# Optimization experiments

Hardware: AMD Instinct MI355X
Metric: run time of the kernel (lower is better)

Reference implementation:

```python
import jax, jax.numpy as jnp
import numpy as np

DIM = 128
B, N = 4, 4096


def setup_inputs() -> dict:
    key = jax.random.key(0)
    k1, k2, k3 = jax.random.split(key, 3)
    return {
        "key": jax.random.normal(k1, (B, N, DIM), dtype=jnp.float32),
        "query": jax.random.normal(k2, (B, N, DIM), dtype=jnp.float32),
        "value": jax.random.normal(k3, (B, N, DIM), dtype=jnp.float32),
    }


def reference(key, query, value):
    # score[b, i, j] = <query[b, i], key[b, j]> / sqrt(dim)
    inv_sqrt_dim = 1.0 / jnp.sqrt(jnp.float32(DIM))
    score = jnp.einsum("bqd,bkd->bqk", query, key) * inv_sqrt_dim
    attn = jax.nn.softmax(score, axis=-1)
    context = jnp.einsum("bqk,bkd->bqd", attn, value)
    return (context, attn)
```

## Files before the change

kernel.cpp:

```cpp
#include <hip/hip_runtime.h>
#include <hip/hip_bf16.h>

#define BDIM 4
#define NSEQ 4096
#define DHEAD 128
#define SCALE 0.08838834764831845f

typedef __bf16 bf16x8 __attribute__((ext_vector_type(8)));
typedef float f32x4 __attribute__((ext_vector_type(4)));

__device__ __forceinline__ unsigned short f2bf(float f){
    return __builtin_bit_cast(unsigned short, (__bf16)f);
}
__device__ __forceinline__ unsigned long long pack4(float4 u){
    return (unsigned long long)f2bf(u.x)
         | ((unsigned long long)f2bf(u.y) << 16)
         | ((unsigned long long)f2bf(u.z) << 32)
         | ((unsigned long long)f2bf(u.w) << 48);
}
__device__ __forceinline__ void gload_lds16(const void* g, void* l){
    __builtin_amdgcn_global_load_lds(
        (const __attribute__((address_space(1))) unsigned int*)g,
        (__attribute__((address_space(3))) unsigned int*)l, 16, 0, 0);
}

extern "C" __global__ __launch_bounds__(256, 4)
void attn_stats(const float* __restrict__ K, const float* __restrict__ Q,
                float* __restrict__ pbase, int pstride)
{
    __shared__ __align__(16) char Klds[64 * 256];

    const int bid = blockIdx.x;
    const int ks  = bid & 3;
    const int rt  = (bid >> 2) & 63;
    const int b   = bid >> 8;
    const int tid = threadIdx.x;
    const int lane = tid & 63;
    const int w    = tid >> 6;
    const int g    = lane >> 4;
    const int c    = lane & 15;
    const int rowbase = rt * 64;

    const float* qrow = Q + ((size_t)b * NSEQ + rowbase + w * 16 + c) * DHEAD;
    bf16x8 qf[4];
#pragma unroll
    for (int kk = 0; kk < 4; kk++) {
        const float4* p0 = (const float4*)(qrow + g * 8 + kk * 32);
        float4 u = p0[0], v = p0[1];
        bf16x8 t;
        t[0] = (__bf16)(u.x * SCALE); t[1] = (__bf16)(u.y * SCALE);
        t[2] = (__bf16)(u.z * SCALE); t[3] = (__bf16)(u.w * SCALE);
        t[4] = (__bf16)(v.x * SCALE); t[5] = (__bf16)(v.y * SCALE);
        t[6] = (__bf16)(v.z * SCALE); t[7] = (__bf16)(v.w * SCALE);
        qf[kk] = t;
    }

    float m[4], l[4];
#pragma unroll
    for (int r = 0; r < 4; r++) { m[r] = -1e30f; l[r] = 0.0f; }

    const int f  = tid & 31;
    const int r0 = tid >> 5;

    for (int kt = 0; kt < 16; kt++) {
        const float* ktile = K + ((size_t)b * NSEQ + ks * 1024 + kt * 64) * DHEAD;
#pragma unroll
        for (int i = 0; i < 8; i++) {
            int r = r0 + i * 8;
            float4 u = *(const float4*)(ktile + (size_t)r * DHEAD + f * 4);
            *(unsigned long long*)(Klds + r * 256 + ((f * 8) ^ ((r & 7) << 4))) = pack4(u);
        }
        __syncthreads();

        f32x4 acc[4];
#pragma unroll
        for (int n = 0; n < 4; n++) acc[n] = (f32x4){0.f, 0.f, 0.f, 0.f};
#pragma unroll
        for (int n = 0; n < 4; n++) {
            int row = n * 16 + c;
#pragma unroll
            for (int kk = 0; kk < 4; kk++) {
                bf16x8 kf = *(const bf16x8*)(Klds + row * 256 +
                                ((g * 16 + kk * 64) ^ ((row & 7) << 4)));
                acc[n] = __builtin_amdgcn_mfma_f32_16x16x32_bf16(qf[kk], kf, acc[n], 0, 0, 0);
            }
        }

#pragma unroll
        for (int r = 0; r < 4; r++) {
            float t = fmaxf(fmaxf(acc[0][r], acc[1][r]), fmaxf(acc[2][r], acc[3][r]));
            t = fmaxf(t, __shfl_xor(t, 1));
            t = fmaxf(t, __shfl_xor(t, 2));
            t = fmaxf(t, __shfl_xor(t, 4));
            t = fmaxf(t, __shfl_xor(t, 8));
            float mn = fmaxf(m[r], t);
            float sc = __expf(m[r] - mn);
            float ps = __expf(acc[0][r] - mn) + __expf(acc[1][r] - mn)
                     + __expf(acc[2][r] - mn) + __expf(acc[3][r] - mn);
            ps += __shfl_xor(ps, 1);
            ps += __shfl_xor(ps, 2);
            ps += __shfl_xor(ps, 4);
            ps += __shfl_xor(ps, 8);
            l[r] = l[r] * sc + ps;
            m[r] = mn;
        }
        __syncthreads();
    }

    if (c == 0) {
#pragma unroll
        for (int r = 0; r < 4; r++) {
            size_t row = rowbase + w * 16 + g * 4 + r;
            float* p = pbase + ((size_t)b * NSEQ + row) * pstride + ks * 2;
            p[0] = m[r];
            p[1] = l[r];
        }
    }
}

extern "C" __global__ __launch_bounds__(256, 4)
void repack(const float* __restrict__ K, const float* __restrict__ V,
            char* __restrict__ ws)
{
    const int bid = blockIdx.x;
    const int T = bid & 63;
    const int b = bid >> 6;
    const int tid = threadIdx.x;

    char* Kp = ws + ((size_t)(b * 64 + T) << 14);
    char* Vp = ws + (4u << 20) + ((size_t)(b * 64 + T) << 14);
    const float* Ks = K + ((size_t)b * NSEQ + T * 64) * DHEAD;
    const float* Vs = V + ((size_t)b * NSEQ + T * 64) * DHEAD;

#pragma unroll
    for (int i = 0; i < 4; i++) {
        int u = tid + 256 * i;
        int row = u >> 4, j = u & 15;
        const float* s = Ks + (size_t)row * DHEAD + (j ^ (row & 7)) * 8;
        float4 a = *(const float4*)s;
        float4 bq = *(const float4*)(s + 4);
        ulonglong2 wv;
        wv.x = pack4(a);
        wv.y = pack4(bq);
        *(ulonglong2*)(Kp + row * 256 + j * 16) = wv;
    }
#pragma unroll
    for (int i = 0; i < 4; i++) {
        int u = tid + 256 * i;
        int d = u >> 3, jj = u & 7;
        int k0 = (jj ^ (d & 7)) * 8;
        float v0 = Vs[(size_t)(k0 + 0) * DHEAD + d];
        float v1 = Vs[(size_t)(k0 + 1) * DHEAD + d];
        float v2 = Vs[(size_t)(k0 + 2) * DHEAD + d];
        float v3 = Vs[(size_t)(k0 + 3) * DHEAD + d];
        float v4 = Vs[(size_t)(k0 + 4) * DHEAD + d];
        float v5 = Vs[(size_t)(k0 + 5) * DHEAD + d];
        float v6 = Vs[(size_t)(k0 + 6) * DHEAD + d];
        float v7 = Vs[(size_t)(k0 + 7) * DHEAD + d];
        ulonglong2 wv;
        wv.x = (unsigned long long)f2bf(v0)
             | ((unsigned long long)f2bf(v1) << 16)
             | ((unsigned long long)f2bf(v2) << 32)
             | ((unsigned long long)f2bf(v3) << 48);
        wv.y = (unsigned long long)f2bf(v4)
             | ((unsigned long long)f2bf(v5) << 16)
             | ((unsigned long long)f2bf(v6) << 32)
             | ((unsigned long long)f2bf(v7) << 48);
        *(ulonglong2*)(Vp + d * 128 + jj * 16) = wv;
    }
}

extern "C" __global__ __launch_bounds__(512, 4)
void attn_final2(const char* __restrict__ ws, const float* __restrict__ Q,
                 float* __restrict__ out)
{
    __shared__ __align__(16) char LDS[73728];

    const int bid = blockIdx.x;
    const int ks  = bid & 1;
    const int rt  = (bid >> 1) & 63;
    const int b   = bid >> 7;
    const int tid = threadIdx.x;
    const int rowbase = rt * 64;
    const int lane = tid & 63;
    const int w    = tid >> 6;
    const int rw   = w & 3;
    const int kh   = w >> 2;
    const int g    = lane >> 4;
    const int c    = lane & 15;

    float* ctxOut = out;
    float* attn   = out + (size_t)BDIM * NSEQ * DHEAD;
    const float* pbase = (const float*)(ws + (8u << 20));

    char* Plds = LDS + 65536 + rw * 2048;

    float Cq;
    {
        const float* prow = pbase + ((size_t)b * NSEQ + rowbase + rw * 16 + c) * 8;
        float4 p0 = *(const float4*)prow;
        float4 p1 = *(const float4*)(prow + 4);
        float M = fmaxf(fmaxf(p0.x, p0.z), fmaxf(p1.x, p1.z));
        float L = p0.y * __expf(p0.x - M) + p0.w * __expf(p0.z - M)
                + p1.y * __expf(p1.x - M) + p1.w * __expf(p1.z - M);
        Cq = M + __logf(L);
    }

    const float* qrow = Q + ((size_t)b * NSEQ + rowbase + rw * 16 + c) * DHEAD;
    bf16x8 qf[4];
#pragma unroll
    for (int kk = 0; kk < 4; kk++) {
        const float4* p0 = (const float4*)(qrow + g * 8 + kk * 32);
        float4 u = p0[0], v = p0[1];
        bf16x8 tt;
        tt[0] = (__bf16)(u.x * SCALE); tt[1] = (__bf16)(u.y * SCALE);
        tt[2] = (__bf16)(u.z * SCALE); tt[3] = (__bf16)(u.w * SCALE);
        tt[4] = (__bf16)(v.x * SCALE); tt[5] = (__bf16)(v.y * SCALE);
        tt[6] = (__bf16)(v.z * SCALE); tt[7] = (__bf16)(v.w * SCALE);
        qf[kk] = tt;
    }

    f32x4 ctx[8];
#pragma unroll
    for (int n2 = 0; n2 < 8; n2++) ctx[n2] = (f32x4){0.f, 0.f, 0.f, 0.f};

    const char* Kg  = ws + ((size_t)(b * 64 + ks * 32) << 14);
    const char* Vg  = ws + (4u << 20) + ((size_t)(b * 64 + ks * 32) << 14);
    const int o0 = tid * 16, o1 = (tid + 512) * 16;

    gload_lds16(Kg + o0, LDS + o0);
    gload_lds16(Kg + o1, LDS + o1);
    gload_lds16(Vg + o0, LDS + 32768 + o0);
    gload_lds16(Vg + o1, LDS + 32768 + o1);

    for (int kt = 0; kt < 32; kt++) {
        __builtin_amdgcn_s_barrier();
        __builtin_amdgcn_sched_barrier(0);
        if (kt < 31) {
            const char* kg = Kg + ((size_t)(kt + 1) << 14);
            const char* vg = Vg + ((size_t)(kt + 1) << 14);
            char* kb = LDS + (((kt + 1) & 1) << 14);
            char* vb = LDS + 32768 + (((kt + 1) & 1) << 14);
            gload_lds16(kg + o0, kb + o0);
            gload_lds16(kg + o1, kb + o1);
            gload_lds16(vg + o0, vb + o0);
            gload_lds16(vg + o1, vb + o1);
            asm volatile("s_waitcnt vmcnt(4)" ::: "memory");
        } else {
            asm volatile("s_waitcnt vmcnt(0)" ::: "memory");
        }
        __builtin_amdgcn_s_barrier();
        __builtin_amdgcn_sched_barrier(0);

        char* Kl = LDS + ((kt & 1) << 14);
        char* Vl = LDS + 32768 + ((kt & 1) << 14);

        f32x4 sacc[2];
#pragma unroll
        for (int nt = 0; nt < 2; nt++) sacc[nt] = (f32x4){0.f, 0.f, 0.f, 0.f};
        __builtin_amdgcn_s_setprio(1);
#pragma unroll
        for (int nt = 0; nt < 2; nt++) {
            int row = kh * 32 + nt * 16 + c;
#pragma unroll
            for (int kk = 0; kk < 4; kk++) {
                bf16x8 kf = *(const bf16x8*)(Kl + row * 256 +
                                ((g * 16 + kk * 64) ^ ((row & 7) << 4)));
                sacc[nt] = __builtin_amdgcn_mfma_f32_16x16x32_bf16(kf, qf[kk], sacc[nt], 0, 0, 0);
            }
        }
        __builtin_amdgcn_s_setprio(0);

        const int col0 = ks * 2048 + kt * 64;
        float* arow = attn + ((size_t)b * NSEQ + rowbase + rw * 16 + c) * NSEQ
                    + col0 + kh * 32;
#pragma unroll
        for (int nt = 0; nt < 2; nt++) {
            float4 pv;
            pv.x = __expf(sacc[nt][0] - Cq);
            pv.y = __expf(sacc[nt][1] - Cq);
            pv.z = __expf(sacc[nt][2] - Cq);
            pv.w = __expf(sacc[nt][3] - Cq);
            *(float4*)(arow + nt * 16 + g * 4) = pv;
            *(unsigned long long*)(Plds + c * 128 +
                ((kh * 64 + nt * 32 + g * 8) ^ ((c & 7) << 4))) = pack4(pv);
        }
        asm volatile("s_waitcnt lgkmcnt(0)" ::: "memory");
        __builtin_amdgcn_sched_barrier(0);

        bf16x8 pf = *(const bf16x8*)(Plds + c * 128 +
                        ((kh * 64 + g * 16) ^ ((c & 7) << 4)));

        __builtin_amdgcn_s_setprio(1);
#pragma unroll
        for (int n2 = 0; n2 < 8; n2++) {
            int d = n2 * 16 + c;
            bf16x8 vf = *(const bf16x8*)(Vl + d * 128 +
                            ((kh * 64 + g * 16) ^ ((d & 7) << 4)));
            ctx[n2] = __builtin_amdgcn_mfma_f32_16x16x32_bf16(pf, vf, ctx[n2], 0, 0, 0);
        }
        __builtin_amdgcn_s_setprio(0);
    }

    __syncthreads();

    float* red = (float*)LDS;
    if (kh == 1) {
#pragma unroll
        for (int n2 = 0; n2 < 8; n2++)
#pragma unroll
            for (int r = 0; r < 4; r++)
                red[(rw * 16 + g * 4 + r) * 128 + n2 * 16 + c] = ctx[n2][r];
    }
    __syncthreads();
    if (kh == 0) {
#pragma unroll
        for (int n2 = 0; n2 < 8; n2++)
#pragma unroll
            for (int r = 0; r < 4; r++) {
                size_t row = rowbase + rw * 16 + g * 4 + r;
                float s = ctx[n2][r] + red[(rw * 16 + g * 4 + r) * 128 + n2 * 16 + c];
                atomicAdd(&ctxOut[((size_t)b * NSEQ + row) * DHEAD + n2 * 16 + c], s);
            }
    }
}

extern "C" __global__ __launch_bounds__(512, 2)
void attn_final_fb(const float* __restrict__ K, const float* __restrict__ Q,
                   const float* __restrict__ V, float* __restrict__ out)
{
    __shared__ __align__(16) char LDS[81920];

    const int bid = blockIdx.x;
    const int rt  = bid & 63;
    const int b   = bid >> 6;
    const int tid = threadIdx.x;
    const int rowbase = rt * 64;
    const int lane = tid & 63;
    const int w    = tid >> 6;
    const int rw   = w & 3;
    const int grp  = w >> 2;
    const int g    = lane >> 4;
    const int c    = lane & 15;
    const int t    = tid & 255;

    float* ctxOut = out;
    float* attn   = out + (size_t)BDIM * NSEQ * DHEAD;

    char* Klds  = LDS + grp * 16384;
    char* Vtlds = LDS + 32768 + grp * 16384;
    char* Plds  = LDS + 65536 + w * 2048;

    float Cq;
    {
        const float* prow = attn + ((size_t)b * NSEQ + rowbase + rw * 16 + c) * NSEQ;
        float4 p0 = *(const float4*)prow;
        float4 p1 = *(const float4*)(prow + 4);
        float M = fmaxf(fmaxf(p0.x, p0.z), fmaxf(p1.x, p1.z));
        float L = p0.y * __expf(p0.x - M) + p0.w * __expf(p0.z - M)
                + p1.y * __expf(p1.x - M) + p1.w * __expf(p1.z - M);
        Cq = M + __logf(L);
    }

    const float* qrow = Q + ((size_t)b * NSEQ + rowbase + rw * 16 + c) * DHEAD;
    bf16x8 qf[4];
#pragma unroll
    for (int kk = 0; kk < 4; kk++) {
        const float4* p0 = (const float4*)(qrow + g * 8 + kk * 32);
        float4 u = p0[0], v = p0[1];
        bf16x8 tt;
        tt[0] = (__bf16)(u.x * SCALE); tt[1] = (__bf16)(u.y * SCALE);
        tt[2] = (__bf16)(u.z * SCALE); tt[3] = (__bf16)(u.w * SCALE);
        tt[4] = (__bf16)(v.x * SCALE); tt[5] = (__bf16)(v.y * SCALE);
        tt[6] = (__bf16)(v.z * SCALE); tt[7] = (__bf16)(v.w * SCALE);
        qf[kk] = tt;
    }

    f32x4 ctx[8];
#pragma unroll
    for (int n2 = 0; n2 < 8; n2++) ctx[n2] = (f32x4){0.f, 0.f, 0.f, 0.f};

    __syncthreads();

    const int fK = t & 31;
    const int rK = t >> 5;
    const int dq = t & 15;
    const int kb = t >> 4;
    const int k0 = kb * 4;
    const int d0 = dq * 2;

    const float* kbase = K + ((size_t)b * NSEQ + grp * 2048) * DHEAD;
    const float* vbase = V + ((size_t)b * NSEQ + grp * 2048) * DHEAD;

    float4 kreg[8];
    float2 vreg[4][4];

#pragma unroll
    for (int i = 0; i < 8; i++)
        kreg[i] = *(const float4*)(kbase + (size_t)(rK + i * 8) * DHEAD + fK * 4);
#pragma unroll
    for (int i = 0; i < 4; i++)
#pragma unroll
        for (int j = 0; j < 4; j++)
            vreg[i][j] = *(const float2*)(vbase + (size_t)(k0 + j) * DHEAD + d0 + 32 * i);

    for (int kt = 0; kt < 32; kt++) {
        __builtin_amdgcn_s_barrier();

#pragma unroll
        for (int i = 0; i < 8; i++) {
            int row = rK + i * 8;
            *(unsigned long long*)(Klds + row * 256 + ((fK * 8) ^ ((row & 7) << 4))) = pack4(kreg[i]);
        }
#pragma unroll
        for (int i = 0; i < 4; i++) {
            int d = d0 + 32 * i;
            unsigned long long rr0 =
                (unsigned long long)f2bf(vreg[i][0].x)
              | ((unsigned long long)f2bf(vreg[i][1].x) << 16)
              | ((unsigned long long)f2bf(vreg[i][2].x) << 32)
              | ((unsigned long long)f2bf(vreg[i][3].x) << 48);
            unsigned long long rr1 =
                (unsigned long long)f2bf(vreg[i][0].y)
              | ((unsigned long long)f2bf(vreg[i][1].y) << 16)
              | ((unsigned long long)f2bf(vreg[i][2].y) << 32)
              | ((unsigned long long)f2bf(vreg[i][3].y) << 48);
            int swz = (d & 7) << 4;
            *(unsigned long long*)(Vtlds + d * 128 + ((k0 * 2) ^ swz)) = rr0;
            *(unsigned long long*)(Vtlds + (d + 1) * 128 + ((k0 * 2) ^ (swz + 16))) = rr1;
        }
        asm volatile("s_waitcnt lgkmcnt(0)" ::: "memory");
        __builtin_amdgcn_s_barrier();

        {
            int kn = (kt + 1) & 31;
            const float* kp = kbase + (size_t)kn * 64 * DHEAD;
            const float* vp = vbase + (size_t)kn * 64 * DHEAD;
#pragma unroll
            for (int i = 0; i < 8; i++)
                kreg[i] = *(const float4*)(kp + (size_t)(rK + i * 8) * DHEAD + fK * 4);
#pragma unroll
            for (int i = 0; i < 4; i++)
#pragma unroll
                for (int j = 0; j < 4; j++)
                    vreg[i][j] = *(const float2*)(vp + (size_t)(k0 + j) * DHEAD + d0 + 32 * i);
        }

        f32x4 sacc[4];
#pragma unroll
        for (int nt = 0; nt < 4; nt++) sacc[nt] = (f32x4){0.f, 0.f, 0.f, 0.f};
        __builtin_amdgcn_s_setprio(1);
#pragma unroll
        for (int nt = 0; nt < 4; nt++) {
            int row = nt * 16 + c;
#pragma unroll
            for (int kk = 0; kk < 4; kk++) {
                bf16x8 kf = *(const bf16x8*)(Klds + row * 256 +
                                ((g * 16 + kk * 64) ^ ((row & 7) << 4)));
                sacc[nt] = __builtin_amdgcn_mfma_f32_16x16x32_bf16(kf, qf[kk], sacc[nt], 0, 0, 0);
            }
        }
        __builtin_amdgcn_s_setprio(0);

        const int col0 = grp * 2048 + kt * 64;
        float* arow = attn + ((size_t)b * NSEQ + rowbase + rw * 16 + c) * NSEQ + col0;
#pragma unroll
        for (int nt = 0; nt < 4; nt++) {
            float4 pv;
            pv.x = __expf(sacc[nt][0] - Cq);
            pv.y = __expf(sacc[nt][1] - Cq);
            pv.z = __expf(sacc[nt][2] - Cq);
            pv.w = __expf(sacc[nt][3] - Cq);
            *(float4*)(arow + nt * 16 + g * 4) = pv;
            *(unsigned long long*)(Plds + c * 128 +
                ((nt * 32 + g * 8) ^ ((c & 7) << 4))) = pack4(pv);
        }
        asm volatile("s_waitcnt lgkmcnt(0)" ::: "memory");
        __builtin_amdgcn_sched_barrier(0);

        bf16x8 pf[2];
#pragma unroll
        for (int kk = 0; kk < 2; kk++)
            pf[kk] = *(const bf16x8*)(Plds + c * 128 +
                        ((kk * 64 + g * 16) ^ ((c & 7) << 4)));

        __builtin_amdgcn_s_setprio(1);
#pragma unroll
        for (int n2 = 0; n2 < 8; n2++) {
            int d = n2 * 16 + c;
#pragma unroll
            for (int kk = 0; kk < 2; kk++) {
                bf16x8 vf = *(const bf16x8*)(Vtlds + d * 128 +
                                ((kk * 64 + g * 16) ^ ((d & 7) << 4)));
                ctx[n2] = __builtin_amdgcn_mfma_f32_16x16x32_bf16(pf[kk], vf, ctx[n2], 0, 0, 0);
            }
        }
        __builtin_amdgcn_s_setprio(0);
    }

    __syncthreads();

    float* red = (float*)LDS;
    if (grp == 1) {
#pragma unroll
        for (int n2 = 0; n2 < 8; n2++)
#pragma unroll
            for (int r = 0; r < 4; r++)
                red[(rw * 16 + g * 4 + r) * 128 + n2 * 16 + c] = ctx[n2][r];
    }
    __syncthreads();
    if (grp == 0) {
#pragma unroll
        for (int n2 = 0; n2 < 8; n2++)
#pragma unroll
            for (int r = 0; r < 4; r++) {
                size_t row = rowbase + rw * 16 + g * 4 + r;
                ctxOut[((size_t)b * NSEQ + row) * DHEAD + n2 * 16 + c] =
                    ctx[n2][r] + red[(rw * 16 + g * 4 + r) * 128 + n2 * 16 + c];
            }
    }
}

extern "C" void kernel_launch(void* const* d_in, const int* in_sizes, int n_in,
                              void* d_out, int out_size, void* d_ws, size_t ws_size,
                              hipStream_t stream)
{
    const float* K = (const float*)d_in[0];
    const float* Q = (const float*)d_in[1];
    const float* V = (const float*)d_in[2];
    float* out  = (float*)d_out;
    float* attn = out + (size_t)BDIM * NSEQ * DHEAD;

    const size_t need = (8u << 20) + (size_t)BDIM * NSEQ * 8 * sizeof(float);
    if (ws_size >= need) {
        char* ws = (char*)d_ws;
        float* pb = (float*)(ws + (8u << 20));
        hipMemsetAsync(out, 0, (size_t)BDIM * NSEQ * DHEAD * sizeof(float), stream);
        attn_stats<<<dim3(4 * 64 * 4), dim3(256), 0, stream>>>(K, Q, pb, 8);
        repack<<<dim3(4 * 64), dim3(256), 0, stream>>>(K, V, ws);
        attn_final2<<<dim3(4 * 64 * 2), dim3(512), 0, stream>>>(ws, Q, out);
    } else {
        attn_stats<<<dim3(4 * 64 * 4), dim3(256), 0, stream>>>(K, Q, attn, NSEQ);
        attn_final_fb<<<dim3(4 * 64), dim3(512), 0, stream>>>(K, Q, V, out);
    }
}
```

Measured before the change: 154.2 us.

## Repack K/V into MFMA fragment order and stream operands directly from global

```diff
diff --git a/kernel.cpp b/kernel.cpp
--- a/kernel.cpp
+++ b/kernel.cpp
@@ -17,11 +17,6 @@
          | ((unsigned long long)f2bf(u.y) << 16)
          | ((unsigned long long)f2bf(u.z) << 32)
          | ((unsigned long long)f2bf(u.w) << 48);
-}
-__device__ __forceinline__ void gload_lds16(const void* g, void* l){
-    __builtin_amdgcn_global_load_lds(
-        (const __attribute__((address_space(1))) unsigned int*)g,
-        (__attribute__((address_space(3))) unsigned int*)l, 16, 0, 0);
 }
 
 extern "C" __global__ __launch_bounds__(256, 4)
@@ -119,8 +114,8 @@
 }
 
 extern "C" __global__ __launch_bounds__(256, 4)
-void repack(const float* __restrict__ K, const float* __restrict__ V,
-            char* __restrict__ ws)
+void repack2(const float* __restrict__ K, const float* __restrict__ V,
+             char* __restrict__ ws)
 {
     const int bid = blockIdx.x;
     const int T = bid & 63;
@@ -135,20 +130,21 @@
 #pragma unroll
     for (int i = 0; i < 4; i++) {
         int u = tid + 256 * i;
-        int row = u >> 4, j = u & 15;
-        const float* s = Ks + (size_t)row * DHEAD + (j ^ (row & 7)) * 8;
+        int t4 = u >> 8, kk = (u >> 6) & 3, g = (u >> 4) & 3, c = u & 15;
+        const float* s = Ks + (size_t)(t4 * 16 + c) * DHEAD + g * 8 + kk * 32;
         float4 a = *(const float4*)s;
         float4 bq = *(const float4*)(s + 4);
         ulonglong2 wv;
         wv.x = pack4(a);
         wv.y = pack4(bq);
-        *(ulonglong2*)(Kp + row * 256 + j * 16) = wv;
+        *(ulonglong2*)(Kp + u * 16) = wv;
     }
 #pragma unroll
     for (int i = 0; i < 4; i++) {
         int u = tid + 256 * i;
-        int d = u >> 3, jj = u & 7;
-        int k0 = (jj ^ (d & 7)) * 8;
+        int n2 = u >> 7, kq = (u >> 6) & 1, g = (u >> 4) & 3, c = u & 15;
+        int d = n2 * 16 + c;
+        int k0 = kq * 32 + g * 8;
         float v0 = Vs[(size_t)(k0 + 0) * DHEAD + d];
         float v1 = Vs[(size_t)(k0 + 1) * DHEAD + d];
         float v2 = Vs[(size_t)(k0 + 2) * DHEAD + d];
@@ -166,15 +162,15 @@
              | ((unsigned long long)f2bf(v5) << 16)
              | ((unsigned long long)f2bf(v6) << 32)
              | ((unsigned long long)f2bf(v7) << 48);
-        *(ulonglong2*)(Vp + d * 128 + jj * 16) = wv;
-    }
-}
-
-extern "C" __global__ __launch_bounds__(512, 4)
-void attn_final2(const char* __restrict__ ws, const float* __restrict__ Q,
+        *(ulonglong2*)(Vp + u * 16) = wv;
+    }
+}
+
+extern "C" __global__ __launch_bounds__(512, 2)
+void attn_stream(const char* __restrict__ ws, const float* __restrict__ Q,
                  float* __restrict__ out)
 {
-    __shared__ __align__(16) char LDS[73728];
+    __shared__ __align__(16) char LDS[32768];
 
     const int bid = blockIdx.x;
     const int ks  = bid & 1;
@@ -184,8 +180,8 @@
     const int rowbase = rt * 64;
     const int lane = tid & 63;
     const int w    = tid >> 6;
-    const int rw   = w & 3;
-    const int kh   = w >> 2;
+    const int kq   = w & 1;
+    const int qh   = w >> 1;
     const int g    = lane >> 4;
     const int c    = lane & 15;
 
@@ -193,11 +189,15 @@
     float* attn   = out + (size_t)BDIM * NSEQ * DHEAD;
     const float* pbase = (const float*)(ws + (8u << 20));
 
-    char* Plds = LDS + 65536 + rw * 2048;
+    char* Pw = LDS + w * 1024;
+    const int swz = ((c >> 2) & 3) << 1;
+    const int pwoff0 = c * 64 + (((0 * 4 + g) ^ swz) << 3);
+    const int pwoff1 = c * 64 + (((1 * 4 + g) ^ swz) << 3);
+    const int proff  = c * 64 + (((2 * g) ^ swz) << 3);
 
     float Cq;
     {
-        const float* prow = pbase + ((size_t)b * NSEQ + rowbase + rw * 16 + c) * 8;
+        const float* prow = pbase + ((size_t)b * NSEQ + rowbase + qh * 16 + c) * 8;
         float4 p0 = *(const float4*)prow;
         float4 p1 = *(const float4*)(prow + 4);
         float M = fmaxf(fmaxf(p0.x, p0.z), fmaxf(p1.x, p1.z));
@@ -206,7 +206,7 @@
         Cq = M + __logf(L);
     }
 
-    const float* qrow = Q + ((size_t)b * NSEQ + rowbase + rw * 16 + c) * DHEAD;
+    const float* qrow = Q + ((size_t)b * NSEQ + rowbase + qh * 16 + c) * DHEAD;
     bf16x8 qf[4];
 #pragma unroll
     for (int kk = 0; kk < 4; kk++) {
@@ -224,102 +224,80 @@
 #pragma unroll
     for (int n2 = 0; n2 < 8; n2++) ctx[n2] = (f32x4){0.f, 0.f, 0.f, 0.f};
 
-    const char* Kg  = ws + ((size_t)(b * 64 + ks * 32) << 14);
-    const char* Vg  = ws + (4u << 20) + ((size_t)(b * 64 + ks * 32) << 14);
-    const int o0 = tid * 16, o1 = (tid + 512) * 16;
-
-    gload_lds16(Kg + o0, LDS + o0);
-    gload_lds16(Kg + o1, LDS + o1);
-    gload_lds16(Vg + o0, LDS + 32768 + o0);
-    gload_lds16(Vg + o1, LDS + 32768 + o1);
-
+    const int loff = g * 256 + c * 16;
+    const char* Kp = ws + ((size_t)(b * 64 + ks * 32) << 14);
+    const char* Vp = ws + (4u << 20) + ((size_t)(b * 64 + ks * 32) << 14);
+    float* arowb = attn + ((size_t)b * NSEQ + rowbase + qh * 16 + c) * NSEQ + ks * 2048;
+
+#pragma unroll 2
     for (int kt = 0; kt < 32; kt++) {
-        __builtin_amdgcn_s_barrier();
-        __builtin_amdgcn_sched_barrier(0);
-        if (kt < 31) {
-            const char* kg = Kg + ((size_t)(kt + 1) << 14);
-            const char* vg = Vg + ((size_t)(kt + 1) << 14);
-            char* kb = LDS + (((kt + 1) & 1) << 14);
-            char* vb = LDS + 32768 + (((kt + 1) & 1) << 14);
-            gload_lds16(kg + o0, kb + o0);
-            gload_lds16(kg + o1, kb + o1);
-            gload_lds16(vg + o0, vb + o0);
-            gload_lds16(vg + o1, vb + o1);
-            asm volatile("s_waitcnt vmcnt(4)" ::: "memory");
-        } else {
-            asm volatile("s_waitcnt vmcnt(0)" ::: "memory");
-        }
-        __builtin_amdgcn_s_barrier();
-        __builtin_amdgcn_sched_barrier(0);
-
-        char* Kl = LDS + ((kt & 1) << 14);
-        char* Vl = LDS + 32768 + ((kt & 1) << 14);
+        const char* kt_base = Kp + ((size_t)kt << 14);
+        const char* vt_base = Vp + ((size_t)kt << 14);
+
+        bf16x8 kf[8];
+#pragma unroll
+        for (int nt = 0; nt < 2; nt++)
+#pragma unroll
+            for (int kk = 0; kk < 4; kk++)
+                kf[nt * 4 + kk] = *(const bf16x8*)(kt_base +
+                    (((kq * 2 + nt) * 4 + kk) << 10) + loff);
+        bf16x8 vf[8];
+#pragma unroll
+        for (int n2 = 0; n2 < 8; n2++)
+            vf[n2] = *(const bf16x8*)(vt_base + ((n2 * 2 + kq) << 10) + loff);
 
         f32x4 sacc[2];
 #pragma unroll
         for (int nt = 0; nt < 2; nt++) sacc[nt] = (f32x4){0.f, 0.f, 0.f, 0.f};
         __builtin_amdgcn_s_setprio(1);
 #pragma unroll
-        for (int nt = 0; nt < 2; nt++) {
-            int row = kh * 32 + nt * 16 + c;
-#pragma unroll
-            for (int kk = 0; kk < 4; kk++) {
-                bf16x8 kf = *(const bf16x8*)(Kl + row * 256 +
-                                ((g * 16 + kk * 64) ^ ((row & 7) << 4)));
-                sacc[nt] = __builtin_amdgcn_mfma_f32_16x16x32_bf16(kf, qf[kk], sacc[nt], 0, 0, 0);
-            }
-        }
+        for (int nt = 0; nt < 2; nt++)
+#pragma unroll
+            for (int kk = 0; kk < 4; kk++)
+                sacc[nt] = __builtin_amdgcn_mfma_f32_16x16x32_bf16(
+                                kf[nt * 4 + kk], qf[kk], sacc[nt], 0, 0, 0);
         __builtin_amdgcn_s_setprio(0);
 
-        const int col0 = ks * 2048 + kt * 64;
-        float* arow = attn + ((size_t)b * NSEQ + rowbase + rw * 16 + c) * NSEQ
-                    + col0 + kh * 32;
-#pragma unroll
-        for (int nt = 0; nt < 2; nt++) {
-            float4 pv;
-            pv.x = __expf(sacc[nt][0] - Cq);
-            pv.y = __expf(sacc[nt][1] - Cq);
-            pv.z = __expf(sacc[nt][2] - Cq);
-            pv.w = __expf(sacc[nt][3] - Cq);
-            *(float4*)(arow + nt * 16 + g * 4) = pv;
-            *(unsigned long long*)(Plds + c * 128 +
-                ((kh * 64 + nt * 32 + g * 8) ^ ((c & 7) << 4))) = pack4(pv);
-        }
+        float* arow = arowb + kt * 64 + kq * 32;
+        float4 pv0, pv1;
+        pv0.x = __expf(sacc[0][0] - Cq); pv0.y = __expf(sacc[0][1] - Cq);
+        pv0.z = __expf(sacc[0][2] - Cq); pv0.w = __expf(sacc[0][3] - Cq);
+        pv1.x = __expf(sacc[1][0] - Cq); pv1.y = __expf(sacc[1][1] - Cq);
+        pv1.z = __expf(sacc[1][2] - Cq); pv1.w = __expf(sacc[1][3] - Cq);
+        *(float4*)(arow + g * 4)      = pv0;
+        *(float4*)(arow + 16 + g * 4) = pv1;
+        *(unsigned long long*)(Pw + pwoff0) = pack4(pv0);
+        *(unsigned long long*)(Pw + pwoff1) = pack4(pv1);
         asm volatile("s_waitcnt lgkmcnt(0)" ::: "memory");
         __builtin_amdgcn_sched_barrier(0);
 
-        bf16x8 pf = *(const bf16x8*)(Plds + c * 128 +
-                        ((kh * 64 + g * 16) ^ ((c & 7) << 4)));
+        bf16x8 pf = *(const bf16x8*)(Pw + proff);
 
         __builtin_amdgcn_s_setprio(1);
 #pragma unroll
-        for (int n2 = 0; n2 < 8; n2++) {
-            int d = n2 * 16 + c;
-            bf16x8 vf = *(const bf16x8*)(Vl + d * 128 +
-                            ((kh * 64 + g * 16) ^ ((d & 7) << 4)));
-            ctx[n2] = __builtin_amdgcn_mfma_f32_16x16x32_bf16(pf, vf, ctx[n2], 0, 0, 0);
-        }
+        for (int n2 = 0; n2 < 8; n2++)
+            ctx[n2] = __builtin_amdgcn_mfma_f32_16x16x32_bf16(pf, vf[n2], ctx[n2], 0, 0, 0);
         __builtin_amdgcn_s_setprio(0);
     }
 
     __syncthreads();
 
     float* red = (float*)LDS;
-    if (kh == 1) {
+    if (kq == 1) {
 #pragma unroll
         for (int n2 = 0; n2 < 8; n2++)
 #pragma unroll
             for (int r = 0; r < 4; r++)
-                red[(rw * 16 + g * 4 + r) * 128 + n2 * 16 + c] = ctx[n2][r];
+                red[(qh * 16 + g * 4 + r) * 128 + n2 * 16 + c] = ctx[n2][r];
     }
     __syncthreads();
-    if (kh == 0) {
+    if (kq == 0) {
 #pragma unroll
         for (int n2 = 0; n2 < 8; n2++)
 #pragma unroll
             for (int r = 0; r < 4; r++) {
-                size_t row = rowbase + rw * 16 + g * 4 + r;
-                float s = ctx[n2][r] + red[(rw * 16 + g * 4 + r) * 128 + n2 * 16 + c];
+                size_t row = rowbase + qh * 16 + g * 4 + r;
+                float s = ctx[n2][r] + red[(qh * 16 + g * 4 + r) * 128 + n2 * 16 + c];
                 atomicAdd(&ctxOut[((size_t)b * NSEQ + row) * DHEAD + n2 * 16 + c], s);
             }
     }
@@ -490,9 +468,9 @@
             int d = n2 * 16 + c;
 #pragma unroll
             for (int kk = 0; kk < 2; kk++) {
-                bf16x8 vf = *(const bf16x8*)(Vtlds + d * 128 +
+                bf16x8 vff = *(const bf16x8*)(Vtlds + d * 128 +
                                 ((kk * 64 + g * 16) ^ ((d & 7) << 4)));
-                ctx[n2] = __builtin_amdgcn_mfma_f32_16x16x32_bf16(pf[kk], vf, ctx[n2], 0, 0, 0);
+                ctx[n2] = __builtin_amdgcn_mfma_f32_16x16x32_bf16(pf[kk], vff, ctx[n2], 0, 0, 0);
             }
         }
         __builtin_amdgcn_s_setprio(0);
@@ -537,8 +515,8 @@
         float* pb = (float*)(ws + (8u << 20));
         hipMemsetAsync(out, 0, (size_t)BDIM * NSEQ * DHEAD * sizeof(float), stream);
         attn_stats<<<dim3(4 * 64 * 4), dim3(256), 0, stream>>>(K, Q, pb, 8);
-        repack<<<dim3(4 * 64), dim3(256), 0, stream>>>(K, V, ws);
-        attn_final2<<<dim3(4 * 64 * 2), dim3(512), 0, stream>>>(ws, Q, out);
+        repack2<<<dim3(4 * 64), dim3(256), 0, stream>>>(K, V, ws);
+        attn_stream<<<dim3(4 * 64 * 2), dim3(512), 0, stream>>>(ws, Q, out);
     } else {
         attn_stats<<<dim3(4 * 64 * 4), dim3(256), 0, stream>>>(K, Q, attn, NSEQ);
         attn_final_fb<<<dim3(4 * 64), dim3(512), 0, stream>>>(K, Q, V, out);
```

New measurement: 183.1 us. 1.19x slower.
